# Kernel tuning notes

Hardware: AMD Instinct MI355X
Metric: run time of the kernel (lower is better)

Reference implementation:

```python
import jax, jax.numpy as jnp
import numpy as np

DIM = 1024
HEADS = 16
B, N = 2, 2048


def setup_inputs() -> dict:
    key = jax.random.key(0)
    ks = jax.random.split(key, 10)
    s = 1.0 / np.sqrt(DIM)
    return {
        "y2_for": jax.random.normal(ks[0], (B, N, DIM), jnp.float32),
        "y2_back": jax.random.normal(ks[1], (B, N, DIM), jnp.float32),
        "Wq": jax.random.normal(ks[2], (DIM, DIM), jnp.float32) * s,
        "bq": jnp.zeros((DIM,), jnp.float32),
        "Wk": jax.random.normal(ks[3], (DIM, DIM), jnp.float32) * s,
        "bk": jnp.zeros((DIM,), jnp.float32),
        "Wv": jax.random.normal(ks[4], (DIM, DIM), jnp.float32) * s,
        "bv": jnp.zeros((DIM,), jnp.float32),
        "Wo": jax.random.normal(ks[5], (DIM, DIM), jnp.float32) * s,
        "bo": jnp.zeros((DIM,), jnp.float32),
    }


def reference(y2_for, y2_back, Wq, bq, Wk, bk, Wv, bv, Wo, bo):
    h = HEADS
    d = DIM // h
    scale = d ** -0.5
    q = y2_for @ Wq + bq                    # [b, n, dim]
    k = y2_back @ Wk + bk
    v = (y2_back + y2_for) @ Wv + bv

    def split_heads(x):
        b, n, _ = x.shape
        return x.reshape(b, n, h, d).transpose(0, 2, 1, 3)  # [b, h, n, d]

    q, k, v = split_heads(q), split_heads(k), split_heads(v)
    attn = jax.nn.softmax(jnp.einsum('bhid,bhjd->bhij', q, k) * scale, axis=-1)
    out = jnp.einsum('bhij,bhjd->bhid', attn, v)
    out = out.transpose(0, 2, 1, 3).reshape(y2_for.shape)   # [b, n, dim]
    out = out + y2_for + y2_back
    return out @ Wo + bo
```

## Files before the change

kernel.cpp:

```cpp
#include <hip/hip_runtime.h>

#define DIM 1024
#define HEADS 16
#define BB 2
#define NN 2048
#define HD 64
#define M_ROWS (BB*NN)

typedef __bf16 bf16x8 __attribute__((ext_vector_type(8)));
typedef float f32x4 __attribute__((ext_vector_type(4)));
typedef short s16x4 __attribute__((ext_vector_type(4)));

__device__ inline unsigned short f2bf(float f) {
    unsigned int u = __builtin_bit_cast(unsigned int, f);
    u += 0x7fffu + ((u >> 16) & 1u);
    return (unsigned short)(u >> 16);
}
__device__ inline float bf2f(unsigned short u) {
    return __builtin_bit_cast(float, (unsigned int)u << 16);
}
__device__ inline bf16x8 as_bf16x8(uint4 v) {
    return __builtin_bit_cast(bf16x8, v);
}
__device__ __forceinline__ void gl_lds16(const unsigned short* g, unsigned short* l) {
    __builtin_amdgcn_global_load_lds(
        (const __attribute__((address_space(1))) unsigned int*)g,
        (__attribute__((address_space(3))) unsigned int*)l, 16, 0, 0);
}

__device__ __forceinline__ f32x4 mfma16x16x16bf16(s16x4 a, s16x4 b, f32x4 c) {
#if __has_builtin(__builtin_amdgcn_mfma_f32_16x16x16bf16_1k)
    return __builtin_amdgcn_mfma_f32_16x16x16bf16_1k(a, b, c, 0, 0, 0);
#else
    asm volatile("v_mfma_f32_16x16x16_bf16 %0, %1, %2, %0"
                 : "+v"(c) : "v"(a), "v"(b));
    return c;
#endif
}

__global__ __launch_bounds__(256) void prep_w(
    const float* __restrict__ Wq, const float* __restrict__ Wk,
    const float* __restrict__ Wv, const float* __restrict__ Wo,
    unsigned short* __restrict__ Wt_all)
{
    __shared__ float tile[32][33];
    const int m = blockIdx.z;
    const float* W = (m == 0) ? Wq : (m == 1) ? Wk : (m == 2) ? Wv : Wo;
    const int bk = blockIdx.x, bn = blockIdx.y;
    const int tx = threadIdx.x & 31, ty = threadIdx.x >> 5;

    #pragma unroll
    for (int i = 0; i < 32; i += 8)
        tile[ty + i][tx] = W[(size_t)(bk*32 + ty + i)*DIM + bn*32 + tx];
    __syncthreads();
    unsigned short* dst = Wt_all + (size_t)m * DIM * DIM;
    #pragma unroll
    for (int i = 0; i < 32; i += 8)
        dst[(size_t)(bn*32 + ty + i)*DIM + bk*32 + tx] = f2bf(tile[tx][ty + i]);
}

__global__ __launch_bounds__(256) void prep_act(
    const float* __restrict__ y2f, const float* __restrict__ y2b,
    unsigned short* __restrict__ Af, unsigned short* __restrict__ Ab,
    unsigned short* __restrict__ As)
{
    const size_t idx = ((size_t)blockIdx.x*256 + threadIdx.x) * 8;
    #pragma unroll
    for (int half = 0; half < 2; half++) {
        float4 f = *(const float4*)(y2f + idx + half*4);
        float4 b = *(const float4*)(y2b + idx + half*4);
        ushort4 of, ob, os;
        of.x = f2bf(f.x); of.y = f2bf(f.y); of.z = f2bf(f.z); of.w = f2bf(f.w);
        ob.x = f2bf(b.x); ob.y = f2bf(b.y); ob.z = f2bf(b.z); ob.w = f2bf(b.w);
        os.x = f2bf(f.x + b.x); os.y = f2bf(f.y + b.y);
        os.z = f2bf(f.z + b.z); os.w = f2bf(f.w + b.w);
        *(ushort4*)(Af + idx + half*4) = of;
        *(ushort4*)(Ab + idx + half*4) = ob;
        *(ushort4*)(As + idx + half*4) = os;
    }
}

__global__ __launch_bounds__(256) void gemm_qkv(
    const unsigned short* __restrict__ Af, const unsigned short* __restrict__ Ab,
    const unsigned short* __restrict__ As,
    const unsigned short* __restrict__ Wt_all,
    const float* __restrict__ bq, const float* __restrict__ bk,
    const float* __restrict__ bv,
    unsigned short* __restrict__ Qh, unsigned short* __restrict__ Kh,
    unsigned short* __restrict__ Vt)
{
    const int bm = blockIdx.x;
    const int mode = blockIdx.y >> 3;
    const int bn = blockIdx.y & 7;
    __shared__ __align__(16) unsigned short sA[128*32];
    __shared__ __align__(16) unsigned short sB[128*32];
    const int t = threadIdx.x;
    const int w = t >> 6, lane = t & 63, ln = lane & 15, quad = lane >> 4;
    const int wm = w >> 1, wn = w & 1;
    const unsigned short* Wt = Wt_all + (size_t)mode * (DIM*DIM);
    const unsigned short* A0 = (mode == 0) ? Af : (mode == 1) ? Ab : As;

    const int srow = lane >> 2;
    const int scol = (lane & 3) * 8;

    f32x4 acc[4][4];
    #pragma unroll
    for (int mi = 0; mi < 4; mi++)
        #pragma unroll
        for (int ni = 0; ni < 4; ni++)
            acc[mi][ni] = (f32x4){0.f, 0.f, 0.f, 0.f};

    for (int kt = 0; kt < 32; kt++) {
        __syncthreads();
        #pragma unroll
        for (int j = 0; j < 2; j++) {
            int row = w*32 + j*16;
            gl_lds16(A0 + (size_t)(bm*128 + row + srow)*DIM + kt*32 + scol,
                     &sA[row*32]);
            gl_lds16(Wt + (size_t)(bn*128 + row + srow)*DIM + kt*32 + scol,
                     &sB[row*32]);
        }
        __syncthreads();

        bf16x8 af[4], bfr[4];
        #pragma unroll
        for (int mi = 0; mi < 4; mi++)
            af[mi] = as_bf16x8(*(const uint4*)(&sA[(wm*64 + mi*16 + ln)*32 + quad*8]));
        #pragma unroll
        for (int ni = 0; ni < 4; ni++)
            bfr[ni] = as_bf16x8(*(const uint4*)(&sB[(wn*64 + ni*16 + ln)*32 + quad*8]));
        #pragma unroll
        for (int mi = 0; mi < 4; mi++)
            #pragma unroll
            for (int ni = 0; ni < 4; ni++)
                acc[mi][ni] = __builtin_amdgcn_mfma_f32_16x16x32_bf16(af[mi], bfr[ni], acc[mi][ni], 0, 0, 0);
    }

    if (mode < 2) {
        const float* bias = (mode == 0) ? bq : bk;
        unsigned short* dst = (mode == 0) ? Qh : Kh;
        const float sc = (mode == 0) ? 0.125f * 1.4426950408889634f : 1.0f;
        #pragma unroll
        for (int mi = 0; mi < 4; mi++) {
            #pragma unroll
            for (int r = 0; r < 4; r++) {
                int grow = bm*128 + wm*64 + mi*16 + quad*4 + r;
                int b_ = grow >> 11, n = grow & (NN - 1);
                #pragma unroll
                for (int ni = 0; ni < 4; ni++) {
                    int gcol = bn*128 + wn*64 + ni*16 + ln;
                    int hh = gcol >> 6, dd = gcol & 63;
                    float val = (acc[mi][ni][r] + bias[gcol]) * sc;
                    dst[(((size_t)(b_*HEADS + hh))*NN + n)*HD + dd] = f2bf(val);
                }
            }
        }
    } else {
        #pragma unroll
        for (int ni = 0; ni < 4; ni++) {
            int gcol = bn*128 + wn*64 + ni*16 + ln;
            int hh = gcol >> 6, dd = gcol & 63;
            float bb = bv[gcol];
            #pragma unroll
            for (int mi = 0; mi < 4; mi++) {
                int grow0 = bm*128 + wm*64 + mi*16 + quad*4;
                int b_ = grow0 >> 11, n0 = grow0 & (NN - 1);
                ushort4 hv;
                hv.x = f2bf(acc[mi][ni][0] + bb);
                hv.y = f2bf(acc[mi][ni][1] + bb);
                hv.z = f2bf(acc[mi][ni][2] + bb);
                hv.w = f2bf(acc[mi][ni][3] + bb);
                *(ushort4*)(Vt + (((size_t)(b_*HEADS + hh))*HD + dd)*NN + n0) = hv;
            }
        }
    }
}

__global__ __launch_bounds__(256) void gemm_out(
    const unsigned short* __restrict__ attp,
    const unsigned short* __restrict__ Wt_all,
    const float* __restrict__ bo, float* __restrict__ out)
{
    const int bm = blockIdx.x, bn = blockIdx.y;
    __shared__ __align__(16) unsigned short sA[64*32];
    __shared__ __align__(16) unsigned short sB[128*32];
    const int t = threadIdx.x;
    const int w = t >> 6, lane = t & 63, ln = lane & 15, quad = lane >> 4;
    const int wm = w >> 1, wn = w & 1;
    const unsigned short* Wt = Wt_all + (size_t)3 * (DIM*DIM);

    const int srow = lane >> 2;
    const int scol = (lane & 3) * 8;

    f32x4 acc[2][4];
    #pragma unroll
    for (int mi = 0; mi < 2; mi++)
        #pragma unroll
        for (int ni = 0; ni < 4; ni++)
            acc[mi][ni] = (f32x4){0.f, 0.f, 0.f, 0.f};

    for (int kt = 0; kt < 32; kt++) {
        __syncthreads();
        gl_lds16(attp + (size_t)(bm*64 + w*16 + srow)*DIM + kt*32 + scol,
                 &sA[(w*16)*32]);
        #pragma unroll
        for (int j = 0; j < 2; j++) {
            int row = w*32 + j*16;
            gl_lds16(Wt + (size_t)(bn*128 + row + srow)*DIM + kt*32 + scol,
                     &sB[row*32]);
        }
        __syncthreads();

        bf16x8 af[2], bfr[4];
        #pragma unroll
        for (int mi = 0; mi < 2; mi++)
            af[mi] = as_bf16x8(*(const uint4*)(&sA[(wm*32 + mi*16 + ln)*32 + quad*8]));
        #pragma unroll
        for (int ni = 0; ni < 4; ni++)
            bfr[ni] = as_bf16x8(*(const uint4*)(&sB[(wn*64 + ni*16 + ln)*32 + quad*8]));
        #pragma unroll
        for (int mi = 0; mi < 2; mi++)
            #pragma unroll
            for (int ni = 0; ni < 4; ni++)
                acc[mi][ni] = __builtin_amdgcn_mfma_f32_16x16x32_bf16(af[mi], bfr[ni], acc[mi][ni], 0, 0, 0);
    }

    #pragma unroll
    for (int mi = 0; mi < 2; mi++) {
        #pragma unroll
        for (int r = 0; r < 4; r++) {
            int grow = bm*64 + wm*32 + mi*16 + quad*4 + r;
            #pragma unroll
            for (int ni = 0; ni < 4; ni++) {
                int gcol = bn*128 + wn*64 + ni*16 + ln;
                out[(size_t)grow*DIM + gcol] = acc[mi][ni][r] + bo[gcol];
            }
        }
    }
}

__global__ __launch_bounds__(256) void attn_kernel(
    const unsigned short* __restrict__ Qh, const unsigned short* __restrict__ Kh,
    const unsigned short* __restrict__ Vt, const unsigned short* __restrict__ As,
    unsigned short* __restrict__ attp)
{
    const int bh = blockIdx.x;
    const int qt = blockIdx.y;
    const int b = bh >> 4, h = bh & 15;
    const int t = threadIdx.x;
    const int w = t >> 6, lane = t & 63, ln = lane & 15, quad = lane >> 4;
    const int sw = ln & 7;
    const float EBIAS = 17.312340490667562f;

    __shared__ __align__(16) unsigned short sK[64*64];
    __shared__ __align__(16) unsigned short sVt[64*64];

    const unsigned short* Qb  = Qh + (size_t)bh * NN * HD + (size_t)qt * 64 * HD;
    const unsigned short* Kb  = Kh + (size_t)bh * NN * HD;
    const unsigned short* Vtb = Vt + (size_t)bh * HD * NN;

    const int rl = lane >> 3, cb = lane & 7;

    #pragma unroll
    for (int j = 0; j < 2; j++) {
        int row = w*16 + j*8 + rl;
        gl_lds16(Qb + (size_t)row*HD + ((cb ^ (row & 7))*8), &sK[(w*16 + j*8)*64]);
    }
    __syncthreads();
    bf16x8 aq[2];
    #pragma unroll
    for (int k = 0; k < 2; k++)
        aq[k] = as_bf16x8(*(const uint4*)(&sK[(w*16 + ln)*64 + (((k*4 + quad) ^ sw)*8)]));

    const s16x4 ones = { (short)0x3F80, (short)0x3F80, (short)0x3F80, (short)0x3F80 };
    f32x4 accO[4], accL;
    accL = (f32x4){0.f, 0.f, 0.f, 0.f};
    #pragma unroll
    for (int di = 0; di < 4; di++) accO[di] = (f32x4){0.f, 0.f, 0.f, 0.f};

    for (int jt = 0; jt < 32; jt++) {
        __syncthreads();
        #pragma unroll
        for (int j = 0; j < 2; j++) {
            int row = w*16 + j*8 + rl;
            gl_lds16(Kb + (size_t)(jt*64 + row)*HD + ((cb ^ (row & 7))*8),
                     &sK[(w*16 + j*8)*64]);
            gl_lds16(Vtb + (size_t)row*NN + jt*64 + ((cb ^ (row & 7))*8),
                     &sVt[(w*16 + j*8)*64]);
        }
        __syncthreads();

        f32x4 accS[4];
        #pragma unroll
        for (int ni = 0; ni < 4; ni++)
            accS[ni] = (f32x4){-EBIAS, -EBIAS, -EBIAS, -EBIAS};
        #pragma unroll
        for (int ni = 0; ni < 4; ni++)
            #pragma unroll
            for (int k = 0; k < 2; k++) {
                bf16x8 bk = as_bf16x8(*(const uint4*)(
                    &sK[(ni*16 + ln)*64 + (((k*4 + quad) ^ sw)*8)]));
                accS[ni] = __builtin_amdgcn_mfma_f32_16x16x32_bf16(bk, aq[k], accS[ni], 0, 0, 0);
            }

        s16x4 pf[4];
        #pragma unroll
        for (int ni = 0; ni < 4; ni++) {
            unsigned int e0 = __builtin_bit_cast(unsigned int, __builtin_amdgcn_exp2f(accS[ni][0]));
            unsigned int e1 = __builtin_bit_cast(unsigned int, __builtin_amdgcn_exp2f(accS[ni][1]));
            unsigned int e2 = __builtin_bit_cast(unsigned int, __builtin_amdgcn_exp2f(accS[ni][2]));
            unsigned int e3 = __builtin_bit_cast(unsigned int, __builtin_amdgcn_exp2f(accS[ni][3]));
            unsigned int lo = __builtin_amdgcn_perm(e1, e0, 0x07060302u);
            unsigned int hi = __builtin_amdgcn_perm(e3, e2, 0x07060302u);
            pf[ni] = __builtin_bit_cast(s16x4, uint2{lo, hi});
            accL = mfma16x16x16bf16(pf[ni], ones, accL);
        }

        #pragma unroll
        for (int ni = 0; ni < 4; ni++) {
            int blkv = 2*ni + (quad >> 1);
            int off = (quad & 1) * 4;
            #pragma unroll
            for (int di = 0; di < 4; di++) {
                s16x4 bv = __builtin_bit_cast(s16x4,
                    *(const uint2*)(&sVt[(di*16 + ln)*64 + ((blkv ^ sw)*8) + off]));
                accO[di] = mfma16x16x16bf16(pf[ni], bv, accO[di]);
            }
        }
    }

    #pragma unroll
    for (int r = 0; r < 4; r++) {
        float inv = 1.f / accL[r];
        int n = qt*64 + w*16 + quad*4 + r;
        #pragma unroll
        for (int di = 0; di < 4; di++) {
            int c = h*64 + di*16 + ln;
            size_t gi = ((size_t)b*NN + n)*DIM + c;
            float o = accO[di][r]*inv + bf2f(As[gi]);
            attp[gi] = f2bf(o);
        }
    }
}

extern "C" void kernel_launch(void* const* d_in, const int* in_sizes, int n_in,
                              void* d_out, int out_size, void* d_ws, size_t ws_size,
                              hipStream_t stream) {
    const float* y2f = (const float*)d_in[0];
    const float* y2b = (const float*)d_in[1];
    const float* Wq  = (const float*)d_in[2];
    const float* bq  = (const float*)d_in[3];
    const float* Wk  = (const float*)d_in[4];
    const float* bk  = (const float*)d_in[5];
    const float* Wv  = (const float*)d_in[6];
    const float* bv  = (const float*)d_in[7];
    const float* Wo  = (const float*)d_in[8];
    const float* bo  = (const float*)d_in[9];
    float* out = (float*)d_out;

    const size_t NACT = (size_t)M_ROWS * DIM;
    unsigned short* ws   = (unsigned short*)d_ws;
    unsigned short* Af   = ws;
    unsigned short* Ab   = ws + NACT;
    unsigned short* As   = ws + 2*NACT;
    unsigned short* Qh   = ws + 3*NACT;
    unsigned short* Kh   = ws + 4*NACT;
    unsigned short* Vt   = ws + 5*NACT;
    unsigned short* Wt   = ws + 6*NACT;
    unsigned short* attp = Ab;

    prep_w<<<dim3(32, 32, 4), 256, 0, stream>>>(Wq, Wk, Wv, Wo, Wt);
    prep_act<<<dim3(2048), 256, 0, stream>>>(y2f, y2b, Af, Ab, As);
    gemm_qkv<<<dim3(32, 24), 256, 0, stream>>>(
        Af, Ab, As, Wt, bq, bk, bv, Qh, Kh, Vt);
    attn_kernel<<<dim3(32, 32), 256, 0, stream>>>(Qh, Kh, Vt, As, attp);
    gemm_out<<<dim3(64, 8), 256, 0, stream>>>(attp, Wt, bo, out);
}
```

Measured before the change: 228.8 us.

## Double-buffer LDS tiles in QKV, output GEMM and attention kernels

Adds a second shared-memory buffer to each of the three kernels. The next K-tile (or K/V tile) is issued into the alternate buffer before the current one is consumed, and the two barriers per iteration become one. The aim is to hide global-to-LDS load latency behind the MFMA work. It doubles LDS use per block, which can lower occupancy, and it depends on the async load being complete by the single barrier.

```diff
diff --git a/kernel.cpp b/kernel.cpp
--- a/kernel.cpp
+++ b/kernel.cpp
@@ -92,8 +92,8 @@
     const int bm = blockIdx.x;
     const int mode = blockIdx.y >> 3;
     const int bn = blockIdx.y & 7;
-    __shared__ __align__(16) unsigned short sA[128*32];
-    __shared__ __align__(16) unsigned short sB[128*32];
+    __shared__ __align__(16) unsigned short sA[2][128*32];
+    __shared__ __align__(16) unsigned short sB[2][128*32];
     const int t = threadIdx.x;
     const int w = t >> 6, lane = t & 63, ln = lane & 15, quad = lane >> 4;
     const int wm = w >> 1, wn = w & 1;
@@ -103,37 +103,44 @@
     const int srow = lane >> 2;
     const int scol = (lane & 3) * 8;
 
-    f32x4 acc[4][4];
-    #pragma unroll
-    for (int mi = 0; mi < 4; mi++)
-        #pragma unroll
-        for (int ni = 0; ni < 4; ni++)
-            acc[mi][ni] = (f32x4){0.f, 0.f, 0.f, 0.f};
-
-    for (int kt = 0; kt < 32; kt++) {
-        __syncthreads();
+    auto stage = [&](int kt, int buf) {
         #pragma unroll
         for (int j = 0; j < 2; j++) {
             int row = w*32 + j*16;
             gl_lds16(A0 + (size_t)(bm*128 + row + srow)*DIM + kt*32 + scol,
-                     &sA[row*32]);
+                     &sA[buf][row*32]);
             gl_lds16(Wt + (size_t)(bn*128 + row + srow)*DIM + kt*32 + scol,
-                     &sB[row*32]);
-        }
-        __syncthreads();
+                     &sB[buf][row*32]);
+        }
+    };
+
+    f32x4 acc[4][4];
+    #pragma unroll
+    for (int mi = 0; mi < 4; mi++)
+        #pragma unroll
+        for (int ni = 0; ni < 4; ni++)
+            acc[mi][ni] = (f32x4){0.f, 0.f, 0.f, 0.f};
+
+    stage(0, 0);
+    __syncthreads();
+
+    for (int kt = 0; kt < 32; kt++) {
+        const int cur = kt & 1;
+        if (kt < 31) stage(kt + 1, cur ^ 1);
 
         bf16x8 af[4], bfr[4];
         #pragma unroll
         for (int mi = 0; mi < 4; mi++)
-            af[mi] = as_bf16x8(*(const uint4*)(&sA[(wm*64 + mi*16 + ln)*32 + quad*8]));
-        #pragma unroll
-        for (int ni = 0; ni < 4; ni++)
-            bfr[ni] = as_bf16x8(*(const uint4*)(&sB[(wn*64 + ni*16 + ln)*32 + quad*8]));
+            af[mi] = as_bf16x8(*(const uint4*)(&sA[cur][(wm*64 + mi*16 + ln)*32 + quad*8]));
+        #pragma unroll
+        for (int ni = 0; ni < 4; ni++)
+            bfr[ni] = as_bf16x8(*(const uint4*)(&sB[cur][(wn*64 + ni*16 + ln)*32 + quad*8]));
         #pragma unroll
         for (int mi = 0; mi < 4; mi++)
             #pragma unroll
             for (int ni = 0; ni < 4; ni++)
                 acc[mi][ni] = __builtin_amdgcn_mfma_f32_16x16x32_bf16(af[mi], bfr[ni], acc[mi][ni], 0, 0, 0);
+        __syncthreads();
     }
 
     if (mode < 2) {
@@ -182,8 +189,8 @@
     const float* __restrict__ bo, float* __restrict__ out)
 {
     const int bm = blockIdx.x, bn = blockIdx.y;
-    __shared__ __align__(16) unsigned short sA[64*32];
-    __shared__ __align__(16) unsigned short sB[128*32];
+    __shared__ __align__(16) unsigned short sA[2][64*32];
+    __shared__ __align__(16) unsigned short sB[2][128*32];
     const int t = threadIdx.x;
     const int w = t >> 6, lane = t & 63, ln = lane & 15, quad = lane >> 4;
     const int wm = w >> 1, wn = w & 1;
@@ -192,37 +199,44 @@
     const int srow = lane >> 2;
     const int scol = (lane & 3) * 8;
 
-    f32x4 acc[2][4];
-    #pragma unroll
-    for (int mi = 0; mi < 2; mi++)
-        #pragma unroll
-        for (int ni = 0; ni < 4; ni++)
-            acc[mi][ni] = (f32x4){0.f, 0.f, 0.f, 0.f};
-
-    for (int kt = 0; kt < 32; kt++) {
-        __syncthreads();
+    auto stage = [&](int kt, int buf) {
         gl_lds16(attp + (size_t)(bm*64 + w*16 + srow)*DIM + kt*32 + scol,
-                 &sA[(w*16)*32]);
+                 &sA[buf][(w*16)*32]);
         #pragma unroll
         for (int j = 0; j < 2; j++) {
             int row = w*32 + j*16;
             gl_lds16(Wt + (size_t)(bn*128 + row + srow)*DIM + kt*32 + scol,
-                     &sB[row*32]);
-        }
-        __syncthreads();
+                     &sB[buf][row*32]);
+        }
+    };
+
+    f32x4 acc[2][4];
+    #pragma unroll
+    for (int mi = 0; mi < 2; mi++)
+        #pragma unroll
+        for (int ni = 0; ni < 4; ni++)
+            acc[mi][ni] = (f32x4){0.f, 0.f, 0.f, 0.f};
+
+    stage(0, 0);
+    __syncthreads();
+
+    for (int kt = 0; kt < 32; kt++) {
+        const int cur = kt & 1;
+        if (kt < 31) stage(kt + 1, cur ^ 1);
 
         bf16x8 af[2], bfr[4];
         #pragma unroll
         for (int mi = 0; mi < 2; mi++)
-            af[mi] = as_bf16x8(*(const uint4*)(&sA[(wm*32 + mi*16 + ln)*32 + quad*8]));
-        #pragma unroll
-        for (int ni = 0; ni < 4; ni++)
-            bfr[ni] = as_bf16x8(*(const uint4*)(&sB[(wn*64 + ni*16 + ln)*32 + quad*8]));
+            af[mi] = as_bf16x8(*(const uint4*)(&sA[cur][(wm*32 + mi*16 + ln)*32 + quad*8]));
+        #pragma unroll
+        for (int ni = 0; ni < 4; ni++)
+            bfr[ni] = as_bf16x8(*(const uint4*)(&sB[cur][(wn*64 + ni*16 + ln)*32 + quad*8]));
         #pragma unroll
         for (int mi = 0; mi < 2; mi++)
             #pragma unroll
             for (int ni = 0; ni < 4; ni++)
                 acc[mi][ni] = __builtin_amdgcn_mfma_f32_16x16x32_bf16(af[mi], bfr[ni], acc[mi][ni], 0, 0, 0);
+        __syncthreads();
     }
 
     #pragma unroll
@@ -252,8 +266,8 @@
     const int sw = ln & 7;
     const float EBIAS = 17.312340490667562f;
 
-    __shared__ __align__(16) unsigned short sK[64*64];
-    __shared__ __align__(16) unsigned short sVt[64*64];
+    __shared__ __align__(16) unsigned short sK[2][64*64];
+    __shared__ __align__(16) unsigned short sV[2][64*64];
 
     const unsigned short* Qb  = Qh + (size_t)bh * NN * HD + (size_t)qt * 64 * HD;
     const unsigned short* Kb  = Kh + (size_t)bh * NN * HD;
@@ -261,16 +275,30 @@
 
     const int rl = lane >> 3, cb = lane & 7;
 
+    auto stageKV = [&](int jt, int buf) {
+        #pragma unroll
+        for (int j = 0; j < 2; j++) {
+            int row = w*16 + j*8 + rl;
+            gl_lds16(Kb + (size_t)(jt*64 + row)*HD + ((cb ^ (row & 7))*8),
+                     &sK[buf][(w*16 + j*8)*64]);
+            gl_lds16(Vtb + (size_t)row*NN + jt*64 + ((cb ^ (row & 7))*8),
+                     &sV[buf][(w*16 + j*8)*64]);
+        }
+    };
+
     #pragma unroll
     for (int j = 0; j < 2; j++) {
         int row = w*16 + j*8 + rl;
-        gl_lds16(Qb + (size_t)row*HD + ((cb ^ (row & 7))*8), &sK[(w*16 + j*8)*64]);
-    }
+        gl_lds16(Qb + (size_t)row*HD + ((cb ^ (row & 7))*8),
+                 &sK[1][(w*16 + j*8)*64]);
+    }
+    stageKV(0, 0);
     __syncthreads();
     bf16x8 aq[2];
     #pragma unroll
     for (int k = 0; k < 2; k++)
-        aq[k] = as_bf16x8(*(const uint4*)(&sK[(w*16 + ln)*64 + (((k*4 + quad) ^ sw)*8)]));
+        aq[k] = as_bf16x8(*(const uint4*)(&sK[1][(w*16 + ln)*64 + (((k*4 + quad) ^ sw)*8)]));
+    __syncthreads();
 
     const s16x4 ones = { (short)0x3F80, (short)0x3F80, (short)0x3F80, (short)0x3F80 };
     f32x4 accO[4], accL;
@@ -279,16 +307,8 @@
     for (int di = 0; di < 4; di++) accO[di] = (f32x4){0.f, 0.f, 0.f, 0.f};
 
     for (int jt = 0; jt < 32; jt++) {
-        __syncthreads();
-        #pragma unroll
-        for (int j = 0; j < 2; j++) {
-            int row = w*16 + j*8 + rl;
-            gl_lds16(Kb + (size_t)(jt*64 + row)*HD + ((cb ^ (row & 7))*8),
-                     &sK[(w*16 + j*8)*64]);
-            gl_lds16(Vtb + (size_t)row*NN + jt*64 + ((cb ^ (row & 7))*8),
-                     &sVt[(w*16 + j*8)*64]);
-        }
-        __syncthreads();
+        const int cur = jt & 1;
+        if (jt < 31) stageKV(jt + 1, cur ^ 1);
 
         f32x4 accS[4];
         #pragma unroll
@@ -299,7 +319,7 @@
             #pragma unroll
             for (int k = 0; k < 2; k++) {
                 bf16x8 bk = as_bf16x8(*(const uint4*)(
-                    &sK[(ni*16 + ln)*64 + (((k*4 + quad) ^ sw)*8)]));
+                    &sK[cur][(ni*16 + ln)*64 + (((k*4 + quad) ^ sw)*8)]));
                 accS[ni] = __builtin_amdgcn_mfma_f32_16x16x32_bf16(bk, aq[k], accS[ni], 0, 0, 0);
             }
 
@@ -323,10 +343,11 @@
             #pragma unroll
             for (int di = 0; di < 4; di++) {
                 s16x4 bv = __builtin_bit_cast(s16x4,
-                    *(const uint2*)(&sVt[(di*16 + ln)*64 + ((blkv ^ sw)*8) + off]));
+                    *(const uint2*)(&sV[cur][(di*16 + ln)*64 + ((blkv ^ sw)*8) + off]));
                 accO[di] = mfma16x16x16bf16(pf[ni], bv, accO[di]);
             }
         }
+        __syncthreads();
     }
 
     #pragma unroll
```

After: 236.7 us. 1.03x slower.
